# Performance work log

Measured on AMD Instinct MI355X. Metric: run time of the kernel, lower is better.

Reference implementation:

```python
import jax, jax.numpy as jnp
import numpy as np

B, S, D, H = 2, 2048, 1024, 16
DK = D // H
NEG = -1.0e9

def setup_inputs() -> dict:
    key = jax.random.key(0)
    ks = jax.random.split(key, 12)
    sc = 1.0 / np.sqrt(D)
    q = jax.random.normal(ks[0], (B, S, D), jnp.float32)
    k = jax.random.normal(ks[1], (B, S, D), jnp.float32)
    v = jax.random.normal(ks[2], (B, S, D), jnp.float32)
    # causal mask: True = masked (matches masked_fill(mask == True, -1e9))
    mask = jnp.broadcast_to(jnp.triu(jnp.ones((S, S), bool), k=1)[None, None], (B, 1, S, S))
    Wq = jax.random.normal(ks[3], (D, D), jnp.float32) * sc
    bq = jnp.zeros((D,), jnp.float32)
    Wk = jax.random.normal(ks[4], (D, D), jnp.float32) * sc
    bk = jnp.zeros((D,), jnp.float32)
    Wv = jax.random.normal(ks[5], (D, D), jnp.float32) * sc
    bv = jnp.zeros((D,), jnp.float32)
    Wo = jax.random.normal(ks[6], (D, D), jnp.float32) * sc
    bo = jnp.zeros((D,), jnp.float32)
    return {"q": q, "k": k, "v": v, "mask": mask,
            "Wq": Wq, "bq": bq, "Wk": Wk, "bk": bk,
            "Wv": Wv, "bv": bv, "Wo": Wo, "bo": bo}

def reference(q, k, v, mask, Wq, bq, Wk, bk, Wv, bv, Wo, bo):
    def split_heads(x):  # [B,S,D] -> [B,H,S,DK]
        return x.reshape(B, S, H, DK).transpose(0, 2, 1, 3)
    qh = split_heads(q @ Wq + bq)
    kh = split_heads(k @ Wk + bk)
    vh = split_heads(v @ Wv + bv)
    scores = jnp.einsum('bhqd,bhkd->bhqk', qh, kh) / np.sqrt(DK)
    scores = jnp.where(mask, NEG, scores)
    p = jax.nn.softmax(scores, axis=-1)
    out = jnp.einsum('bhqk,bhkd->bhqd', p, vh)  # [B,H,S,DK]
    out = out.transpose(0, 2, 1, 3).reshape(B, S, D)
    return out @ Wo + bo
```

## Files before the change

kernel.cpp:

```cpp
#include <hip/hip_runtime.h>

#define BB 2
#define SS 2048
#define DD 1024
#define HH 16
#define DKK 64

typedef __attribute__((ext_vector_type(8))) short short8;
typedef __attribute__((ext_vector_type(4))) float floatx4;

__device__ inline float bf2f(ushort u) {
    union { unsigned int i; float f; } x; x.i = ((unsigned int)u) << 16; return x.f;
}
__device__ inline ushort f2bf(float f) {
    union { float f; unsigned int i; } x; x.f = f;
    unsigned int r = x.i + 0x7fff + ((x.i >> 16) & 1);
    return (ushort)(r >> 16);
}
__device__ inline void async_cp16(const ushort* g, ushort* l) {
    __builtin_amdgcn_global_load_lds(
        (const __attribute__((address_space(1))) unsigned int*)g,
        (__attribute__((address_space(3))) unsigned int*)l, 16, 0, 0);
}

__global__ __launch_bounds__(256) void cvt_w4(const float* __restrict__ w0,
                                              const float* __restrict__ w1,
                                              const float* __restrict__ w2,
                                              const float* __restrict__ w3,
                                              ushort* __restrict__ o0,
                                              ushort* __restrict__ o1,
                                              ushort* __restrict__ o2,
                                              ushort* __restrict__ o3) {
    __shared__ ushort t[32][33];
    int z = blockIdx.z;
    const float* in = (z == 0) ? w0 : (z == 1) ? w1 : (z == 2) ? w2 : w3;
    ushort* out = (z == 0) ? o0 : (z == 1) ? o1 : (z == 2) ? o2 : o3;
    int bx = blockIdx.x, by = blockIdx.y, tx = threadIdx.x;
    for (int i = threadIdx.y; i < 32; i += 8)
        t[i][tx] = f2bf(in[(size_t)(by * 32 + i) * DD + bx * 32 + tx]);
    __syncthreads();
    for (int i = threadIdx.y; i < 32; i += 8)
        out[(size_t)(bx * 32 + i) * DD + by * 32 + tx] = t[tx][i];
}

__global__ __launch_bounds__(256) void cvt_qkv(const float* __restrict__ q,
                                               const float* __restrict__ k,
                                               const float* __restrict__ v,
                                               ushort* __restrict__ oq,
                                               ushort* __restrict__ ok,
                                               ushort* __restrict__ ov) {
    int z = blockIdx.z;
    const float* in = (z == 0) ? q : (z == 1) ? k : v;
    ushort* out = (z == 0) ? oq : (z == 1) ? ok : ov;
    int i = blockIdx.x * 256 + threadIdx.x;
    float4 f0 = ((const float4*)in)[i * 2];
    float4 f1 = ((const float4*)in)[i * 2 + 1];
    short8 p;
    p[0] = (short)f2bf(f0.x); p[1] = (short)f2bf(f0.y);
    p[2] = (short)f2bf(f0.z); p[3] = (short)f2bf(f0.w);
    p[4] = (short)f2bf(f1.x); p[5] = (short)f2bf(f1.y);
    p[6] = (short)f2bf(f1.z); p[7] = (short)f2bf(f1.w);
    ((short8*)out)[i] = p;
}

__global__ __launch_bounds__(256) void gemm_qkv(const ushort* __restrict__ Xq,
                                                const ushort* __restrict__ Xk,
                                                const ushort* __restrict__ Xv,
                                                const ushort* __restrict__ WtQ,
                                                const ushort* __restrict__ WtK,
                                                const ushort* __restrict__ WtV,
                                                const float* __restrict__ bq,
                                                const float* __restrict__ bk,
                                                const float* __restrict__ bv,
                                                ushort* __restrict__ qh,
                                                ushort* __restrict__ kh,
                                                ushort* __restrict__ vt) {
    constexpr int K = 1024;
    constexpr int LDT = 136;
    __shared__ ushort smem[128 * LDT];
    ushort* Asm = smem;
    ushort* Bsm = smem + 4096;

    int lin = blockIdx.x + ((blockIdx.y + (blockIdx.z << 5)) << 3);
    int wid = (lin & 7) * 96 + (lin >> 3);
    int z = wid >> 8;
    int rem = wid & 255;
    int by = rem >> 3, bx = rem & 7;

    const ushort* A  = (z == 0) ? Xq : (z == 1) ? Xk : Xv;
    const ushort* Bt = (z == 0) ? WtQ : (z == 1) ? WtK : WtV;
    const float* bias = (z == 0) ? bq : (z == 1) ? bk : bv;
    ushort* outp = (z == 0) ? qh : (z == 1) ? kh : vt;

    int tid = threadIdx.x;
    int wave = tid >> 6, lane = tid & 63, quad = lane >> 4, l15 = lane & 15;
    int wm = wave >> 1, wn = wave & 1;
    int rowBase = by * 128, colBase = bx * 128;

    floatx4 acc[4][4] = {};
    for (int k0 = 0; k0 < K; k0 += 32) {
#pragma unroll
        for (int j = 0; j < 2; ++j) {
            int cbase = (j * 4 + wave) * 64;
            int c = cbase + lane;
            int row = c >> 2, sub = (c & 3) * 8;
            async_cp16(&A[(size_t)(rowBase + row) * K + k0 + sub], &Asm[cbase * 8]);
            async_cp16(&Bt[(size_t)(colBase + row) * K + k0 + sub], &Bsm[cbase * 8]);
        }
        __syncthreads();
        short8 af[4], bf[4];
#pragma unroll
        for (int mi = 0; mi < 4; ++mi)
            af[mi] = *(const short8*)&Asm[(wm * 64 + mi * 16 + l15) * 32 + quad * 8];
#pragma unroll
        for (int ni = 0; ni < 4; ++ni)
            bf[ni] = *(const short8*)&Bsm[(wn * 64 + ni * 16 + l15) * 32 + quad * 8];
#pragma unroll
        for (int mi = 0; mi < 4; ++mi)
#pragma unroll
            for (int ni = 0; ni < 4; ++ni)
                acc[mi][ni] = __builtin_amdgcn_mfma_f32_16x16x32_bf16(
                    af[mi], bf[ni], acc[mi][ni], 0, 0, 0);
        __syncthreads();
    }
    if (z == 2) {
        for (int mi = 0; mi < 4; ++mi)
            for (int ni = 0; ni < 4; ++ni) {
                int c = wn * 64 + ni * 16 + l15;
                float bv = bias[colBase + c];
                for (int i = 0; i < 4; ++i) {
                    int r = wm * 64 + mi * 16 + quad * 4 + i;
                    smem[c * LDT + r] = f2bf(acc[mi][ni][i] + bv);
                }
            }
        __syncthreads();
        int b = rowBase >> 11;
        int sBase = rowBase & 2047;
#pragma unroll
        for (int u = 0; u < 8; ++u) {
            int chunk = u * 256 + tid;
            int c = chunk >> 4;
            int r = (chunk & 15) * 8;
            int col = colBase + c, h = col >> 6, dk = col & 63;
            int4 val = *(const int4*)&smem[c * LDT + r];
            *(int4*)&outp[((size_t)((b * HH + h) * DKK + dk)) * SS + sBase + r] = val;
        }
    } else {
        for (int mi = 0; mi < 4; ++mi)
            for (int ni = 0; ni < 4; ++ni) {
                int c = wn * 64 + ni * 16 + l15;
                float bv = bias[colBase + c];
                for (int i = 0; i < 4; ++i) {
                    int r = wm * 64 + mi * 16 + quad * 4 + i;
                    smem[r * LDT + c] = f2bf(acc[mi][ni][i] + bv);
                }
            }
        __syncthreads();
        int bb = rowBase >> 11;
        int sBase = rowBase & 2047;
#pragma unroll
        for (int u = 0; u < 8; ++u) {
            int chunk = u * 256 + tid;
            int r = chunk >> 4;
            int cc = (chunk & 15) * 8;
            int col = colBase + cc, hh = col >> 6, dk = col & 63;
            int4 val = *(const int4*)&smem[r * LDT + cc];
            *(int4*)&outp[((size_t)((bb * HH + hh) * SS + sBase + r)) * DKK + dk] = val;
        }
    }
}

__global__ __launch_bounds__(256) void gemm_fin(const ushort* __restrict__ A,
                                                const ushort* __restrict__ Bt,
                                                const float* __restrict__ bias,
                                                float* __restrict__ outp) {
    constexpr int K = 1024, N = 1024;
    __shared__ ushort Asm[64 * 32];
    __shared__ ushort Bsm[128 * 32];
    int tid = threadIdx.x;
    int wave = tid >> 6, lane = tid & 63, quad = lane >> 4, l15 = lane & 15;
    int wm = wave >> 1, wn = wave & 1;

    int lin = blockIdx.x + (blockIdx.y << 3);
    int wid = (lin & 7) * 64 + (lin >> 3);
    int bx = wid & 7, by = wid >> 3;
    int rowBase = by * 64, colBase = bx * 128;

    floatx4 acc[2][4] = {};
    for (int k0 = 0; k0 < K; k0 += 32) {
#pragma unroll
        for (int j = 0; j < 3; ++j) {
            int c = j * 4 + wave;
            int cbase = (c < 4) ? c * 64 : (c - 4) * 64;
            int cc = cbase + lane;
            int row = cc >> 2, sub = (cc & 3) * 8;
            if (c < 4)
                async_cp16(&A[(size_t)(rowBase + row) * K + k0 + sub], &Asm[cbase * 8]);
            else
                async_cp16(&Bt[(size_t)(colBase + row) * K + k0 + sub], &Bsm[cbase * 8]);
        }
        __syncthreads();
        short8 af[2], bf[4];
#pragma unroll
        for (int mi = 0; mi < 2; ++mi)
            af[mi] = *(const short8*)&Asm[(wm * 32 + mi * 16 + l15) * 32 + quad * 8];
#pragma unroll
        for (int ni = 0; ni < 4; ++ni)
            bf[ni] = *(const short8*)&Bsm[(wn * 64 + ni * 16 + l15) * 32 + quad * 8];
#pragma unroll
        for (int mi = 0; mi < 2; ++mi)
#pragma unroll
            for (int ni = 0; ni < 4; ++ni)
                acc[mi][ni] = __builtin_amdgcn_mfma_f32_16x16x32_bf16(
                    af[mi], bf[ni], acc[mi][ni], 0, 0, 0);
        __syncthreads();
    }
    for (int mi = 0; mi < 2; ++mi)
        for (int ni = 0; ni < 4; ++ni) {
            int col = colBase + wn * 64 + ni * 16 + l15;
            float bv = bias[col];
            for (int i = 0; i < 4; ++i) {
                int row = rowBase + wm * 32 + mi * 16 + quad * 4 + i;
                outp[(size_t)row * N + col] = acc[mi][ni][i] + bv;
            }
        }
}

__global__ __launch_bounds__(256, 2) void flash_attn4(const ushort* __restrict__ qh,
                                                      const ushort* __restrict__ kh,
                                                      const ushort* __restrict__ vt,
                                                      ushort* __restrict__ attn) {
    constexpr int LD = 72;
    __shared__ ushort Ksm[2][64 * LD];
    __shared__ ushort Vsm[2][64 * LD];
    __shared__ ushort Psm[64 * LD];
    int tid = threadIdx.x;
    int h = blockIdx.y, b = blockIdx.z;
    int wave = tid >> 6, lane = tid & 63, quad = lane >> 4, l15 = lane & 15;
    const size_t headQK = ((size_t)(b * HH + h)) * SS * DKK;
    const size_t headV  = ((size_t)(b * HH + h)) * DKK * SS;
    int c0 = tid, r0 = c0 >> 3, s0 = (c0 & 7) * 8;
    int c1 = tid + 256, r1 = c1 >> 3, s1 = (c1 & 7) * 8;
    const int qt0 = blockIdx.x;
    const int qt1 = 31 - qt0;

    int qrow0 = qt0 * 64 + wave * 16 + l15;
    int qrow1 = qt1 * 64 + wave * 16 + l15;
    short8 q0a = *(const short8*)&qh[headQK + (size_t)qrow0 * DKK + quad * 8];
    short8 q0b = *(const short8*)&qh[headQK + (size_t)qrow0 * DKK + 32 + quad * 8];
    short8 q1a = *(const short8*)&qh[headQK + (size_t)qrow1 * DKK + quad * 8];
    short8 q1b = *(const short8*)&qh[headQK + (size_t)qrow1 * DKK + 32 + quad * 8];

    floatx4 o0[4] = {}, o1[4] = {};
    float l0[4] = {0.f, 0.f, 0.f, 0.f}, l1[4] = {0.f, 0.f, 0.f, 0.f};

    *(int4*)&Ksm[0][r0 * LD + s0] = *(const int4*)&kh[headQK + (size_t)r0 * DKK + s0];
    *(int4*)&Ksm[0][r1 * LD + s1] = *(const int4*)&kh[headQK + (size_t)r1 * DKK + s1];
    *(int4*)&Vsm[0][r0 * LD + s0] = *(const int4*)&vt[headV + (size_t)r0 * SS + s0];
    *(int4*)&Vsm[0][r1 * LD + s1] = *(const int4*)&vt[headV + (size_t)r1 * SS + s1];
    __syncthreads();

    for (int kt = 0; kt <= qt1; ++kt) {
        int cur = kt & 1;
        bool pre = (kt < qt1);
        bool act0 = (kt <= qt0);
        int4 kA, kB, vA, vB;
        if (pre) {
            const ushort* kp = &kh[headQK + (size_t)((kt + 1) * 64) * DKK];
            const ushort* vp = &vt[headV + (kt + 1) * 64];
            kA = *(const int4*)&kp[(size_t)r0 * DKK + s0];
            kB = *(const int4*)&kp[(size_t)r1 * DKK + s1];
            vA = *(const int4*)&vp[(size_t)r0 * SS + s0];
            vB = *(const int4*)&vp[(size_t)r1 * SS + s1];
        }
        floatx4 sv1[4], sv0[4];
#pragma unroll
        for (int cn = 0; cn < 4; ++cn) {
            short8 kf0 = *(const short8*)&Ksm[cur][(cn * 16 + l15) * LD + quad * 8];
            short8 kf1 = *(const short8*)&Ksm[cur][(cn * 16 + l15) * LD + 32 + quad * 8];
            floatx4 z = {};
            z = __builtin_amdgcn_mfma_f32_16x16x32_bf16(q1a, kf0, z, 0, 0, 0);
            z = __builtin_amdgcn_mfma_f32_16x16x32_bf16(q1b, kf1, z, 0, 0, 0);
            sv1[cn] = z;
            if (act0) {
                floatx4 y = {};
                y = __builtin_amdgcn_mfma_f32_16x16x32_bf16(q0a, kf0, y, 0, 0, 0);
                y = __builtin_amdgcn_mfma_f32_16x16x32_bf16(q0b, kf1, y, 0, 0, 0);
                sv0[cn] = y;
            }
        }
        short8 vf[2][4];
#pragma unroll
        for (int ks = 0; ks < 2; ++ks)
#pragma unroll
            for (int n = 0; n < 4; ++n)
                vf[ks][n] = *(const short8*)&Vsm[cur][(n * 16 + l15) * LD + ks * 32 + quad * 8];

        {
            bool diag = (kt == qt1);
#pragma unroll
            for (int cn = 0; cn < 4; ++cn) {
                int colg = kt * 64 + cn * 16 + l15;
#pragma unroll
                for (int i = 0; i < 4; ++i) {
                    float p = __expf(sv1[cn][i] * 0.125f);
                    if (diag) {
                        int rowg = qt1 * 64 + wave * 16 + quad * 4 + i;
                        if (colg > rowg) p = 0.f;
                    }
                    sv1[cn][i] = p;
                    l1[i] += p;
                }
            }
#pragma unroll
            for (int cn = 0; cn < 4; ++cn)
#pragma unroll
                for (int i = 0; i < 4; ++i)
                    Psm[(wave * 16 + quad * 4 + i) * LD + cn * 16 + l15] = f2bf(sv1[cn][i]);
#pragma unroll
            for (int ks = 0; ks < 2; ++ks) {
                short8 pf = *(const short8*)&Psm[(wave * 16 + l15) * LD + ks * 32 + quad * 8];
#pragma unroll
                for (int n = 0; n < 4; ++n)
                    o1[n] = __builtin_amdgcn_mfma_f32_16x16x32_bf16(pf, vf[ks][n], o1[n], 0, 0, 0);
            }
        }
        if (act0) {
            bool diag = (kt == qt0);
#pragma unroll
            for (int cn = 0; cn < 4; ++cn) {
                int colg = kt * 64 + cn * 16 + l15;
#pragma unroll
                for (int i = 0; i < 4; ++i) {
                    float p = __expf(sv0[cn][i] * 0.125f);
                    if (diag) {
                        int rowg = qt0 * 64 + wave * 16 + quad * 4 + i;
                        if (colg > rowg) p = 0.f;
                    }
                    sv0[cn][i] = p;
                    l0[i] += p;
                }
            }
#pragma unroll
            for (int cn = 0; cn < 4; ++cn)
#pragma unroll
                for (int i = 0; i < 4; ++i)
                    Psm[(wave * 16 + quad * 4 + i) * LD + cn * 16 + l15] = f2bf(sv0[cn][i]);
#pragma unroll
            for (int ks = 0; ks < 2; ++ks) {
                short8 pf = *(const short8*)&Psm[(wave * 16 + l15) * LD + ks * 32 + quad * 8];
#pragma unroll
                for (int n = 0; n < 4; ++n)
                    o0[n] = __builtin_amdgcn_mfma_f32_16x16x32_bf16(pf, vf[ks][n], o0[n], 0, 0, 0);
            }
        }
        if (pre) {
            int nb = cur ^ 1;
            *(int4*)&Ksm[nb][r0 * LD + s0] = kA;
            *(int4*)&Ksm[nb][r1 * LD + s1] = kB;
            *(int4*)&Vsm[nb][r0 * LD + s0] = vA;
            *(int4*)&Vsm[nb][r1 * LD + s1] = vB;
        }
        __syncthreads();
    }
#pragma unroll
    for (int i = 0; i < 4; ++i) {
        float a = l0[i], c = l1[i];
        a += __shfl_xor(a, 1, 64); a += __shfl_xor(a, 2, 64);
        a += __shfl_xor(a, 4, 64); a += __shfl_xor(a, 8, 64);
        c += __shfl_xor(c, 1, 64); c += __shfl_xor(c, 2, 64);
        c += __shfl_xor(c, 4, 64); c += __shfl_xor(c, 8, 64);
        l0[i] = a; l1[i] = c;
    }
#pragma unroll
    for (int n = 0; n < 4; ++n)
#pragma unroll
        for (int i = 0; i < 4; ++i) {
            int rg0 = qt0 * 64 + wave * 16 + quad * 4 + i;
            attn[((size_t)(b * SS + rg0)) * DD + h * 64 + n * 16 + l15] =
                f2bf(o0[n][i] / l0[i]);
            int rg1 = qt1 * 64 + wave * 16 + quad * 4 + i;
            attn[((size_t)(b * SS + rg1)) * DD + h * 64 + n * 16 + l15] =
                f2bf(o1[n][i] / l1[i]);
        }
}

extern "C" void kernel_launch(void* const* d_in, const int* in_sizes, int n_in,
                              void* d_out, int out_size, void* d_ws, size_t ws_size,
                              hipStream_t stream) {
    const float* q  = (const float*)d_in[0];
    const float* k  = (const float*)d_in[1];
    const float* v  = (const float*)d_in[2];
    const float* Wq = (const float*)d_in[4];
    const float* bq = (const float*)d_in[5];
    const float* Wk = (const float*)d_in[6];
    const float* bk = (const float*)d_in[7];
    const float* Wv = (const float*)d_in[8];
    const float* bv = (const float*)d_in[9];
    const float* Wo = (const float*)d_in[10];
    const float* bo = (const float*)d_in[11];

    ushort* ws   = (ushort*)d_ws;
    ushort* WtQ  = ws;
    ushort* WtK  = WtQ + (1u << 20);
    ushort* WtV  = WtK + (1u << 20);
    ushort* WtO  = WtV + (1u << 20);
    ushort* Xv   = WtO + (1u << 20);
    ushort* qh   = Xv + (4u << 20);
    ushort* kh   = qh + (4u << 20);
    ushort* vt   = kh + (4u << 20);
    ushort* Xq   = (ushort*)d_out;
    ushort* Xk   = Xq + (4u << 20);
    ushort* attn = Xv;

    cvt_w4<<<dim3(32, 32, 4), dim3(32, 8), 0, stream>>>(Wq, Wk, Wv, Wo,
                                                        WtQ, WtK, WtV, WtO);
    cvt_qkv<<<dim3(2048, 1, 3), 256, 0, stream>>>(q, k, v, Xq, Xk, Xv);

    gemm_qkv<<<dim3(8, 32, 3), 256, 0, stream>>>(Xq, Xk, Xv, WtQ, WtK, WtV,
                                                 bq, bk, bv, qh, kh, vt);

    flash_attn4<<<dim3(16, 16, 2), 256, 0, stream>>>(qh, kh, vt, attn);

    gemm_fin<<<dim3(8, 64), 256, 0, stream>>>(attn, WtO, bo, (float*)d_out);
}
```

Measured before the change: 257.3 us.

## Compute transposed scores and feed P to MFMA via register permutes, dropping LDS staging

Swaps the MFMA operand order so each lane holds scores for one query row (S^T and O^T layouts). The probabilities are packed to bf16 with v_cvt_pk_bf16_f32 and rearranged with permlane32/16 swaps into the B-operand layout, replacing the per-tile round trip through the shared P buffer. The row-sum reduction and output stores are simplified to packed vector writes. This removes LDS traffic and scalar conversions, but relies on gfx950-specific permlane semantics for correctness.

```diff
diff --git a/kernel.cpp b/kernel.cpp
--- a/kernel.cpp
+++ b/kernel.cpp
@@ -21,6 +21,17 @@
     __builtin_amdgcn_global_load_lds(
         (const __attribute__((address_space(1))) unsigned int*)g,
         (__attribute__((address_space(3))) unsigned int*)l, 16, 0, 0);
+}
+__device__ inline unsigned int cvt_pk_bf16(float lo, float hi) {
+    unsigned int r;
+    asm("v_cvt_pk_bf16_f32 %0, %1, %2" : "=v"(r) : "v"(lo), "v"(hi));
+    return r;
+}
+__device__ inline void swap32(unsigned int& a, unsigned int& b) {
+    asm("v_permlane32_swap_b32 %0, %1" : "+v"(a), "+v"(b));
+}
+__device__ inline void swap16(unsigned int& a, unsigned int& b) {
+    asm("v_permlane16_swap_b32 %0, %1" : "+v"(a), "+v"(b));
 }
 
 __global__ __launch_bounds__(256) void cvt_w4(const float* __restrict__ w0,
@@ -226,14 +237,13 @@
         }
 }
 
-__global__ __launch_bounds__(256, 2) void flash_attn4(const ushort* __restrict__ qh,
+__global__ __launch_bounds__(256, 2) void flash_attn5(const ushort* __restrict__ qh,
                                                       const ushort* __restrict__ kh,
                                                       const ushort* __restrict__ vt,
                                                       ushort* __restrict__ attn) {
     constexpr int LD = 72;
     __shared__ ushort Ksm[2][64 * LD];
     __shared__ ushort Vsm[2][64 * LD];
-    __shared__ ushort Psm[64 * LD];
     int tid = threadIdx.x;
     int h = blockIdx.y, b = blockIdx.z;
     int wave = tid >> 6, lane = tid & 63, quad = lane >> 4, l15 = lane & 15;
@@ -252,7 +262,8 @@
     short8 q1b = *(const short8*)&qh[headQK + (size_t)qrow1 * DKK + 32 + quad * 8];
 
     floatx4 o0[4] = {}, o1[4] = {};
-    float l0[4] = {0.f, 0.f, 0.f, 0.f}, l1[4] = {0.f, 0.f, 0.f, 0.f};
+    float l0 = 0.f, l1 = 0.f;
+    int qsel = wave * 16 + l15;
 
     *(int4*)&Ksm[0][r0 * LD + s0] = *(const int4*)&kh[headQK + (size_t)r0 * DKK + s0];
     *(int4*)&Ksm[0][r1 * LD + s1] = *(const int4*)&kh[headQK + (size_t)r1 * DKK + s1];
@@ -279,13 +290,13 @@
             short8 kf0 = *(const short8*)&Ksm[cur][(cn * 16 + l15) * LD + quad * 8];
             short8 kf1 = *(const short8*)&Ksm[cur][(cn * 16 + l15) * LD + 32 + quad * 8];
             floatx4 z = {};
-            z = __builtin_amdgcn_mfma_f32_16x16x32_bf16(q1a, kf0, z, 0, 0, 0);
-            z = __builtin_amdgcn_mfma_f32_16x16x32_bf16(q1b, kf1, z, 0, 0, 0);
+            z = __builtin_amdgcn_mfma_f32_16x16x32_bf16(kf0, q1a, z, 0, 0, 0);
+            z = __builtin_amdgcn_mfma_f32_16x16x32_bf16(kf1, q1b, z, 0, 0, 0);
             sv1[cn] = z;
             if (act0) {
                 floatx4 y = {};
-                y = __builtin_amdgcn_mfma_f32_16x16x32_bf16(q0a, kf0, y, 0, 0, 0);
-                y = __builtin_amdgcn_mfma_f32_16x16x32_bf16(q0b, kf1, y, 0, 0, 0);
+                y = __builtin_amdgcn_mfma_f32_16x16x32_bf16(kf0, q0a, y, 0, 0, 0);
+                y = __builtin_amdgcn_mfma_f32_16x16x32_bf16(kf1, q0b, y, 0, 0, 0);
                 sv0[cn] = y;
             }
         }
@@ -298,60 +309,60 @@
 
         {
             bool diag = (kt == qt1);
+            unsigned int pkd[4][2];
 #pragma unroll
             for (int cn = 0; cn < 4; ++cn) {
-                int colg = kt * 64 + cn * 16 + l15;
 #pragma unroll
                 for (int i = 0; i < 4; ++i) {
                     float p = __expf(sv1[cn][i] * 0.125f);
-                    if (diag) {
-                        int rowg = qt1 * 64 + wave * 16 + quad * 4 + i;
-                        if (colg > rowg) p = 0.f;
-                    }
+                    if (diag && (cn * 16 + quad * 4 + i) > qsel) p = 0.f;
                     sv1[cn][i] = p;
-                    l1[i] += p;
+                    l1 += p;
                 }
-            }
-#pragma unroll
-            for (int cn = 0; cn < 4; ++cn)
-#pragma unroll
-                for (int i = 0; i < 4; ++i)
-                    Psm[(wave * 16 + quad * 4 + i) * LD + cn * 16 + l15] = f2bf(sv1[cn][i]);
+                pkd[cn][0] = cvt_pk_bf16(sv1[cn][0], sv1[cn][1]);
+                pkd[cn][1] = cvt_pk_bf16(sv1[cn][2], sv1[cn][3]);
+            }
 #pragma unroll
             for (int ks = 0; ks < 2; ++ks) {
-                short8 pf = *(const short8*)&Psm[(wave * 16 + l15) * LD + ks * 32 + quad * 8];
+                unsigned int a0 = pkd[ks * 2][0], b0 = pkd[ks * 2 + 1][0];
+                swap32(a0, b0); swap16(a0, b0);
+                unsigned int a1 = pkd[ks * 2][1], b1 = pkd[ks * 2 + 1][1];
+                swap32(a1, b1); swap16(a1, b1);
+                union { int4 i4; short8 s8; } u;
+                u.i4 = make_int4((int)a0, (int)a1, (int)b0, (int)b1);
 #pragma unroll
                 for (int n = 0; n < 4; ++n)
-                    o1[n] = __builtin_amdgcn_mfma_f32_16x16x32_bf16(pf, vf[ks][n], o1[n], 0, 0, 0);
+                    o1[n] = __builtin_amdgcn_mfma_f32_16x16x32_bf16(
+                        vf[ks][n], u.s8, o1[n], 0, 0, 0);
             }
         }
         if (act0) {
             bool diag = (kt == qt0);
+            unsigned int pkd[4][2];
 #pragma unroll
             for (int cn = 0; cn < 4; ++cn) {
-                int colg = kt * 64 + cn * 16 + l15;
 #pragma unroll
                 for (int i = 0; i < 4; ++i) {
                     float p = __expf(sv0[cn][i] * 0.125f);
-                    if (diag) {
-                        int rowg = qt0 * 64 + wave * 16 + quad * 4 + i;
-                        if (colg > rowg) p = 0.f;
-                    }
+                    if (diag && (cn * 16 + quad * 4 + i) > qsel) p = 0.f;
                     sv0[cn][i] = p;
-                    l0[i] += p;
+                    l0 += p;
                 }
-            }
-#pragma unroll
-            for (int cn = 0; cn < 4; ++cn)
-#pragma unroll
-                for (int i = 0; i < 4; ++i)
-                    Psm[(wave * 16 + quad * 4 + i) * LD + cn * 16 + l15] = f2bf(sv0[cn][i]);
+                pkd[cn][0] = cvt_pk_bf16(sv0[cn][0], sv0[cn][1]);
+                pkd[cn][1] = cvt_pk_bf16(sv0[cn][2], sv0[cn][3]);
+            }
 #pragma unroll
             for (int ks = 0; ks < 2; ++ks) {
-                short8 pf = *(const short8*)&Psm[(wave * 16 + l15) * LD + ks * 32 + quad * 8];
+                unsigned int a0 = pkd[ks * 2][0], b0 = pkd[ks * 2 + 1][0];
+                swap32(a0, b0); swap16(a0, b0);
+                unsigned int a1 = pkd[ks * 2][1], b1 = pkd[ks * 2 + 1][1];
+                swap32(a1, b1); swap16(a1, b1);
+                union { int4 i4; short8 s8; } u;
+                u.i4 = make_int4((int)a0, (int)a1, (int)b0, (int)b1);
 #pragma unroll
                 for (int n = 0; n < 4; ++n)
-                    o0[n] = __builtin_amdgcn_mfma_f32_16x16x32_bf16(pf, vf[ks][n], o0[n], 0, 0, 0);
+                    o0[n] = __builtin_amdgcn_mfma_f32_16x16x32_bf16(
+                        vf[ks][n], u.s8, o0[n], 0, 0, 0);
             }
         }
         if (pre) {
@@ -363,26 +374,22 @@
         }
         __syncthreads();
     }
-#pragma unroll
-    for (int i = 0; i < 4; ++i) {
-        float a = l0[i], c = l1[i];
-        a += __shfl_xor(a, 1, 64); a += __shfl_xor(a, 2, 64);
-        a += __shfl_xor(a, 4, 64); a += __shfl_xor(a, 8, 64);
-        c += __shfl_xor(c, 1, 64); c += __shfl_xor(c, 2, 64);
-        c += __shfl_xor(c, 4, 64); c += __shfl_xor(c, 8, 64);
-        l0[i] = a; l1[i] = c;
+    l0 += __shfl_xor(l0, 16, 64); l0 += __shfl_xor(l0, 32, 64);
+    l1 += __shfl_xor(l1, 16, 64); l1 += __shfl_xor(l1, 32, 64);
+    float inv0 = 1.0f / l0, inv1 = 1.0f / l1;
+    size_t rowOff0 = ((size_t)(b * SS + qt0 * 64 + wave * 16 + l15)) * DD + h * 64;
+    size_t rowOff1 = ((size_t)(b * SS + qt1 * 64 + wave * 16 + l15)) * DD + h * 64;
+#pragma unroll
+    for (int n = 0; n < 4; ++n) {
+        int dof = n * 16 + quad * 4;
+        int2 v0, v1;
+        v0.x = (int)cvt_pk_bf16(o0[n][0] * inv0, o0[n][1] * inv0);
+        v0.y = (int)cvt_pk_bf16(o0[n][2] * inv0, o0[n][3] * inv0);
+        v1.x = (int)cvt_pk_bf16(o1[n][0] * inv1, o1[n][1] * inv1);
+        v1.y = (int)cvt_pk_bf16(o1[n][2] * inv1, o1[n][3] * inv1);
+        *(int2*)&attn[rowOff0 + dof] = v0;
+        *(int2*)&attn[rowOff1 + dof] = v1;
     }
-#pragma unroll
-    for (int n = 0; n < 4; ++n)
-#pragma unroll
-        for (int i = 0; i < 4; ++i) {
-            int rg0 = qt0 * 64 + wave * 16 + quad * 4 + i;
-            attn[((size_t)(b * SS + rg0)) * DD + h * 64 + n * 16 + l15] =
-                f2bf(o0[n][i] / l0[i]);
-            int rg1 = qt1 * 64 + wave * 16 + quad * 4 + i;
-            attn[((size_t)(b * SS + rg1)) * DD + h * 64 + n * 16 + l15] =
-                f2bf(o1[n][i] / l1[i]);
-        }
 }
 
 extern "C" void kernel_launch(void* const* d_in, const int* in_sizes, int n_in,
@@ -420,7 +427,7 @@
     gemm_qkv<<<dim3(8, 32, 3), 256, 0, stream>>>(Xq, Xk, Xv, WtQ, WtK, WtV,
                                                  bq, bk, bv, qh, kh, vt);
 
-    flash_attn4<<<dim3(16, 16, 2), 256, 0, stream>>>(qh, kh, vt, attn);
+    flash_attn5<<<dim3(16, 16, 2), 256, 0, stream>>>(qh, kh, vt, attn);
 
     gemm_fin<<<dim3(8, 64), 256, 0, stream>>>(attn, WtO, bo, (float*)d_out);
 }
```

New measurement: 251.0 us. -2.4%, faster.
